# Kernel optimization log

Hardware: AMD Instinct MI355X
Metric: run time of the kernel (lower is better)

## Reference

```python
import jax, jax.numpy as jnp
import numpy as np

EMBED_DIM = 1024
N_HEADS = 16
HEAD_DIM = EMBED_DIM // N_HEADS
B, N = 4, 2048


def setup_inputs() -> dict:
    key = jax.random.key(0)
    k1, k2, k3, k4, k5 = jax.random.split(key, 5)
    x = jax.random.normal(k1, (B, N, EMBED_DIM), dtype=jnp.float32)
    # Per-head kqv Linear weights stacked: torch Linear(embed_dim, 3*head_dim)
    # torch stores weight as [out, in]; we store transposed [in, out] per head.
    scale = 1.0 / np.sqrt(EMBED_DIM)
    W_kqv = jax.random.uniform(k2, (N_HEADS, EMBED_DIM, 3 * HEAD_DIM), dtype=jnp.float32, minval=-scale, maxval=scale)
    b_kqv = jax.random.uniform(k3, (N_HEADS, 3 * HEAD_DIM), dtype=jnp.float32, minval=-scale, maxval=scale)
    W_proj = jax.random.uniform(k4, (EMBED_DIM, EMBED_DIM), dtype=jnp.float32, minval=-scale, maxval=scale)
    b_proj = jax.random.uniform(k5, (EMBED_DIM,), dtype=jnp.float32, minval=-scale, maxval=scale)
    return {"x": x, "W_kqv": W_kqv, "b_kqv": b_kqv, "W_proj": W_proj, "b_proj": b_proj}


def reference(x, W_kqv, b_kqv, W_proj, b_proj):
    Bx, Nx, D = x.shape
    H = W_kqv.shape[0]
    hd = W_kqv.shape[2] // 3
    # All per-head kqv projections at once: [B, H, N, 3*hd]
    kqv = jnp.einsum('bnd,hde->bhne', x, W_kqv) + b_kqv[None, :, None, :]
    # chunk order in source is (k, q, v)
    k, q, v = jnp.split(kqv, 3, axis=-1)
    # scores scaled by sqrt(head_dim) (D1 in attention_scores is head dim)
    scores = jnp.einsum('bhqd,bhkd->bhqk', q, k) / jnp.sqrt(jnp.float32(hd))
    causal = jnp.tril(jnp.ones((Nx, Nx), dtype=bool))  # [N, N]
    scores = jnp.where(causal[None, None, :, :], scores, -jnp.inf)
    attn = jax.nn.softmax(scores, axis=-1)
    sa = jnp.einsum('bhqk,bhkd->bhqd', attn, v)  # [B, H, N, hd]
    # concat heads along feature dim (head order preserved)
    sa = sa.transpose(0, 2, 1, 3).reshape(Bx, Nx, H * hd)
    # output projection: torch Linear with weight [out, in] -> y = sa @ W^T + b;
    # here W_proj is stored as [in, out]
    return sa @ W_proj + b_proj
```

## Files before the change

kernel.cpp:

```cpp
#include <hip/hip_runtime.h>
#include <math.h>

#define EMBED   1024
#define NHEADS  16
#define HD      64
#define BATCH   4
#define SEQ     2048
#define MROWS   (BATCH*SEQ)
#define NKV     8388608ull

typedef short short8 __attribute__((ext_vector_type(8)));
typedef float floatx4 __attribute__((ext_vector_type(4)));

__device__ __forceinline__ unsigned short f2b(float f) {
    union { float f; unsigned u; } v; v.f = f;
    unsigned r = v.u + 0x7FFFu + ((v.u >> 16) & 1u);
    return (unsigned short)(r >> 16);
}
__device__ __forceinline__ unsigned short f2b_fast(float f) {
    union { float f; unsigned u; } v; v.f = f;
    return (unsigned short)((v.u + 0x8000u) >> 16);
}

#define GLDS16(gp, lp) __builtin_amdgcn_global_load_lds( \
    (const __attribute__((address_space(1))) unsigned int*)(gp), \
    (__attribute__((address_space(3))) unsigned int*)(lp), 16, 0, 0)

__global__ __launch_bounds__(256) void convert_x(
    const float* __restrict__ x, unsigned short* __restrict__ x16)
{
    size_t idx = ((size_t)blockIdx.x * 256 + threadIdx.x) * 8;
    float4 a = *(const float4*)(x + idx);
    float4 b = *(const float4*)(x + idx + 4);
    ushort4 u0, u1;
    u0.x = f2b(a.x); u0.y = f2b(a.y); u0.z = f2b(a.z); u0.w = f2b(a.w);
    u1.x = f2b(b.x); u1.y = f2b(b.y); u1.z = f2b(b.z); u1.w = f2b(b.w);
    *(ushort4*)(x16 + idx) = u0;
    *(ushort4*)(x16 + idx + 4) = u1;
}

__global__ __launch_bounds__(256) void prep_wkqv(
    const float* __restrict__ Wk, unsigned short* __restrict__ Wt)
{
    __shared__ float tile[32][33];
    const int h = blockIdx.z;
    const int k0 = blockIdx.x * 32, e0 = blockIdx.y * 32;
    const float* inh = Wk + (size_t)h * 1024 * 192;
    const int tx = threadIdx.x & 31, ty = threadIdx.x >> 5;
    #pragma unroll
    for (int i = 0; i < 4; i++)
        tile[ty + i * 8][tx] = inh[(size_t)(k0 + ty + i * 8) * 192 + e0 + tx];
    __syncthreads();
    #pragma unroll
    for (int i = 0; i < 4; i++) {
        int e = e0 + ty + i * 8;
        int cp = (e >> 6) * 1024 + h * 64 + (e & 63);
        Wt[(size_t)cp * 1024 + k0 + tx] = f2b(tile[tx][ty + i * 8]);
    }
}

__global__ __launch_bounds__(256) void transpose_w(
    const float* __restrict__ in, unsigned short* __restrict__ outp, int R, int C)
{
    __shared__ float tile[32][33];
    const int r0 = blockIdx.x * 32, c0 = blockIdx.y * 32;
    const int tx = threadIdx.x & 31, ty = threadIdx.x >> 5;
    #pragma unroll
    for (int i = 0; i < 4; i++)
        tile[ty + i * 8][tx] = in[(size_t)(r0 + ty + i * 8) * C + c0 + tx];
    __syncthreads();
    #pragma unroll
    for (int i = 0; i < 4; i++)
        outp[(size_t)(c0 + ty + i * 8) * R + r0 + tx] = f2b(tile[tx][ty + i * 8]);
}

__global__ __launch_bounds__(256) void gemm_kqv(
    const unsigned short* __restrict__ A,
    const unsigned short* __restrict__ Bt,
    const float* __restrict__ bk,
    unsigned short* __restrict__ Kb16,
    unsigned short* __restrict__ Qb16,
    unsigned short* __restrict__ Vt16)
{
    __shared__ unsigned short smem[16384];
    unsigned short* As = smem;
    unsigned short* Bs = smem + 8192;

    const int mt = blockIdx.x;
    const int ct = blockIdx.y;
    const int t = threadIdx.x;
    const int wave = t >> 6, lane = t & 63;
    const int lr = lane & 15, quad = lane >> 4;
    const int wm = wave >> 1, wn = wave & 1;
    const int row0 = mt * 128, col0 = ct * 128;
    const int sr = lane >> 3, sc = lane & 7;

    floatx4 acc[4][4];
    #pragma unroll
    for (int a = 0; a < 4; a++)
        #pragma unroll
        for (int n = 0; n < 4; n++) acc[a][n] = (floatx4){0.f, 0.f, 0.f, 0.f};

    for (int k0 = 0; k0 < 1024; k0 += 64) {
        __syncthreads();
        #pragma unroll
        for (int i = 0; i < 4; i++) {
            int q = wave + i * 4;
            GLDS16(A  + (size_t)(row0 + q * 8 + sr) * 1024 + k0 + sc * 8, As + q * 512);
            GLDS16(Bt + (size_t)(col0 + q * 8 + sr) * 1024 + k0 + sc * 8, Bs + q * 512);
        }
        __syncthreads();
        #pragma unroll
        for (int kc = 0; kc < 2; kc++) {
            short8 af[4], bf[4];
            #pragma unroll
            for (int i = 0; i < 4; i++) {
                af[i] = *(const short8*)(As + (wm * 64 + i * 16 + lr) * 64 + kc * 32 + quad * 8);
                bf[i] = *(const short8*)(Bs + (wn * 64 + i * 16 + lr) * 64 + kc * 32 + quad * 8);
            }
            #pragma unroll
            for (int a = 0; a < 4; a++)
                #pragma unroll
                for (int n = 0; n < 4; n++)
                    acc[a][n] = __builtin_amdgcn_mfma_f32_16x16x32_bf16(af[a], bf[n], acc[a][n], 0, 0, 0);
        }
    }

    const int sec = ct >> 3;
    float bias[4];
    #pragma unroll
    for (int n = 0; n < 4; n++) {
        int c = col0 + wn * 64 + n * 16 + lr;
        int h = (c & 1023) >> 6;
        int e = sec * 64 + (c & 63);
        bias[n] = bk[h * 192 + e];
    }
    const int b = row0 >> 11;
    const int n0 = row0 & 2047;
    const float scl = (sec == 1) ? (0.125f * 1.44269504089f) : 1.0f;

    __syncthreads();
    if (sec < 2) {
        #pragma unroll
        for (int a = 0; a < 4; a++)
            #pragma unroll
            for (int n = 0; n < 4; n++) {
                int colS = (wn * 64 + n * 16 + lr) ^ (quad << 4);
                #pragma unroll
                for (int r = 0; r < 4; r++) {
                    int rw = wm * 64 + a * 16 + quad * 4 + r;
                    smem[rw * 128 + colS] = f2b((acc[a][n][r] + bias[n]) * scl);
                }
            }
        __syncthreads();
        unsigned short* dstbuf = (sec == 0) ? Kb16 : Qb16;
        const int rw = t >> 1, half = t & 1;
        const int h2 = (ct & 7) * 2 + half;
        const int s = (rw >> 2) & 3;
        unsigned short* dst = dstbuf + ((size_t)(b * 16 + h2) * 2048 + n0 + rw) * 64;
        #pragma unroll
        for (int u = 0; u < 8; u++) {
            int cg = half * 64 + ((u * 8) ^ (s << 4));
            *(float4*)(dst + u * 8) = *(const float4*)(&smem[rw * 128 + cg]);
        }
    } else {
        #pragma unroll
        for (int a = 0; a < 4; a++)
            #pragma unroll
            for (int n = 0; n < 4; n++) {
                int colv = wn * 64 + n * 16 + lr;
                int rowb = (wm * 64 + a * 16 + quad * 4) ^ ((colv & 7) << 3);
                ushort4 pk;
                pk.x = f2b(acc[a][n][0] + bias[n]);
                pk.y = f2b(acc[a][n][1] + bias[n]);
                pk.z = f2b(acc[a][n][2] + bias[n]);
                pk.w = f2b(acc[a][n][3] + bias[n]);
                *(ushort4*)(&smem[colv * 128 + rowb]) = pk;
            }
        __syncthreads();
        const int cg = t >> 1, hf = t & 1;
        const int d = cg & 63, h2 = (ct & 7) * 2 + (cg >> 6);
        unsigned short* dst = Vt16 + ((size_t)(b * 16 + h2) * 64 + d) * 2048 + n0 + hf * 64;
        #pragma unroll
        for (int u = 0; u < 8; u++) {
            int rr = hf * 64 + u * 8;
            int rs = rr ^ ((cg & 7) << 3);
            *(float4*)(dst + u * 8) = *(const float4*)(&smem[cg * 128 + rs]);
        }
    }
}

__global__ __launch_bounds__(256, 2) void attn_mfma(
    const unsigned short* __restrict__ Kb,
    const unsigned short* __restrict__ Qb,
    const unsigned short* __restrict__ Vt,
    unsigned short* __restrict__ sa)
{
    const int bx = blockIdx.x;
    const int bh = blockIdx.y;
    const int b = bh >> 4, h = bh & 15;
    const int wave = threadIdx.x >> 6;
    const int lane = threadIdx.x & 63;
    const int lr = lane & 15, quad = lane >> 4;
    const int qt_[2] = {bx, 15 - bx};

    __shared__ unsigned short Ks[64 * 64];
    __shared__ unsigned short Vs[64 * 64];
    __shared__ unsigned short Ps[4][2][16 * 72];

    const unsigned short* Kbh = Kb + (size_t)bh * 2048 * 64;
    const unsigned short* Vbh = Vt + (size_t)bh * 64 * 2048;
    const unsigned short* Qbh = Qb + (size_t)bh * 2048 * 64;

    short8 qf[2][2][2];
    #pragma unroll
    for (int tt = 0; tt < 2; tt++)
        #pragma unroll
        for (int s = 0; s < 2; s++) {
            const unsigned short* qp = Qbh +
                (size_t)(qt_[tt] * 128 + wave * 32 + s * 16 + lr) * 64 + quad * 8;
            qf[tt][s][0] = *(const short8*)(qp);
            qf[tt][s][1] = *(const short8*)(qp + 32);
        }

    floatx4 O[2][2][4];
    float ls[2][2][4];
    #pragma unroll
    for (int tt = 0; tt < 2; tt++)
        #pragma unroll
        for (int s = 0; s < 2; s++) {
            #pragma unroll
            for (int d = 0; d < 4; d++) O[tt][s][d] = (floatx4){0.f, 0.f, 0.f, 0.f};
            #pragma unroll
            for (int r = 0; r < 4; r++) ls[tt][s][r] = 0.f;
        }

    const int r_local = lane >> 3, cc = lane & 7;
    const int swz = cc ^ r_local;
    const int whalf = wave >> 1;

    const int ktmax = 2 * qt_[1] + 1;
    for (int kt = 0; kt <= ktmax; kt++) {
        const int k0 = kt * 64;
        __syncthreads();
        #pragma unroll
        for (int j = 0; j < 2; j++) {
            int R = wave * 16 + j * 8 + r_local;
            GLDS16(Kbh + (size_t)(k0 + R) * 64 + swz * 8, Ks + (wave * 16 + j * 8) * 64 + lane * 8);
            GLDS16(Vbh + (size_t)R * 2048 + k0 + swz * 8, Vs + (wave * 16 + j * 8) * 64 + lane * 8);
        }
        __syncthreads();

        #pragma unroll
        for (int tt = 0; tt < 2; tt++) {
            const int qt2 = qt_[tt];
            const int lim = 2 * qt2 + whalf;
            if (kt > lim) continue;

            floatx4 S[2][4];
            #pragma unroll
            for (int s = 0; s < 2; s++)
                #pragma unroll
                for (int a = 0; a < 4; a++) S[s][a] = (floatx4){0.f, 0.f, 0.f, 0.f};
            #pragma unroll
            for (int c = 0; c < 2; c++)
                #pragma unroll
                for (int a = 0; a < 4; a++) {
                    int R = a * 16 + lr;
                    short8 kf = *(const short8*)(Ks + R * 64 + (((c * 4 + quad) ^ (lr & 7)) * 8));
                    #pragma unroll
                    for (int s = 0; s < 2; s++)
                        S[s][a] = __builtin_amdgcn_mfma_f32_16x16x32_bf16(qf[tt][s][c], kf, S[s][a], 0, 0, 0);
                }

            if (kt == lim) {
                #pragma unroll
                for (int s = 0; s < 2; s++)
                    #pragma unroll
                    for (int a = 0; a < 4; a++) {
                        int col = k0 + a * 16 + lr;
                        #pragma unroll
                        for (int r = 0; r < 4; r++) {
                            int grow = qt2 * 128 + wave * 32 + s * 16 + quad * 4 + r;
                            if (col > grow) S[s][a][r] = -INFINITY;
                        }
                    }
            }

            #pragma unroll
            for (int s = 0; s < 2; s++)
                #pragma unroll
                for (int a = 0; a < 4; a++)
                    #pragma unroll
                    for (int r = 0; r < 4; r++) {
                        float p = __builtin_amdgcn_exp2f(S[s][a][r]);
                        ls[tt][s][r] += p;
                        Ps[wave][s][(quad * 4 + r) * 72 + a * 16 + lr] = f2b_fast(p);
                    }

            short8 pa[2][2];
            #pragma unroll
            for (int s = 0; s < 2; s++)
                #pragma unroll
                for (int c = 0; c < 2; c++)
                    pa[s][c] = *(const short8*)(Ps[wave][s] + lr * 72 + c * 32 + quad * 8);

            #pragma unroll
            for (int c = 0; c < 2; c++)
                #pragma unroll
                for (int d = 0; d < 4; d++) {
                    int R = d * 16 + lr;
                    short8 vf = *(const short8*)(Vs + R * 64 + (((c * 4 + quad) ^ (lr & 7)) * 8));
                    #pragma unroll
                    for (int s = 0; s < 2; s++)
                        O[tt][s][d] = __builtin_amdgcn_mfma_f32_16x16x32_bf16(pa[s][c], vf, O[tt][s][d], 0, 0, 0);
                }
        }
    }

    #pragma unroll
    for (int tt = 0; tt < 2; tt++)
        #pragma unroll
        for (int s = 0; s < 2; s++)
            #pragma unroll
            for (int r = 0; r < 4; r++) {
                float sm = ls[tt][s][r];
                sm += __shfl_xor(sm, 1);
                sm += __shfl_xor(sm, 2);
                sm += __shfl_xor(sm, 4);
                sm += __shfl_xor(sm, 8);
                float inv = 1.0f / sm;
                size_t base = ((size_t)(b * 2048 + qt_[tt] * 128 + wave * 32 + s * 16 + quad * 4 + r)) * 1024
                              + h * 64 + lr;
                #pragma unroll
                for (int d = 0; d < 4; d++)
                    sa[base + d * 16] = f2b(O[tt][s][d][r] * inv);
            }
}

__global__ __launch_bounds__(256) void gemm_proj(
    const unsigned short* __restrict__ A,
    const unsigned short* __restrict__ Bt,
    const float* __restrict__ bp,
    float* __restrict__ out)
{
    __shared__ unsigned short smem[16384];
    unsigned short* As = smem;
    unsigned short* Bs = smem + 8192;

    const int mt = blockIdx.x;
    const int ct = blockIdx.y;
    const int t = threadIdx.x;
    const int wave = t >> 6, lane = t & 63;
    const int lr = lane & 15, quad = lane >> 4;
    const int wm = wave >> 1, wn = wave & 1;
    const int row0 = mt * 128, col0 = ct * 128;
    const int sr = lane >> 3, sc = lane & 7;

    floatx4 acc[4][4];
    #pragma unroll
    for (int a = 0; a < 4; a++)
        #pragma unroll
        for (int n = 0; n < 4; n++) acc[a][n] = (floatx4){0.f, 0.f, 0.f, 0.f};

    for (int k0 = 0; k0 < 1024; k0 += 64) {
        __syncthreads();
        #pragma unroll
        for (int i = 0; i < 4; i++) {
            int q = wave + i * 4;
            GLDS16(A  + (size_t)(row0 + q * 8 + sr) * 1024 + k0 + sc * 8, As + q * 512);
            GLDS16(Bt + (size_t)(col0 + q * 8 + sr) * 1024 + k0 + sc * 8, Bs + q * 512);
        }
        __syncthreads();
        #pragma unroll
        for (int kc = 0; kc < 2; kc++) {
            short8 af[4], bf[4];
            #pragma unroll
            for (int i = 0; i < 4; i++) {
                af[i] = *(const short8*)(As + (wm * 64 + i * 16 + lr) * 64 + kc * 32 + quad * 8);
                bf[i] = *(const short8*)(Bs + (wn * 64 + i * 16 + lr) * 64 + kc * 32 + quad * 8);
            }
            #pragma unroll
            for (int a = 0; a < 4; a++)
                #pragma unroll
                for (int n = 0; n < 4; n++)
                    acc[a][n] = __builtin_amdgcn_mfma_f32_16x16x32_bf16(af[a], bf[n], acc[a][n], 0, 0, 0);
        }
    }

    float bias[4]; int cols[4];
    #pragma unroll
    for (int n = 0; n < 4; n++) {
        cols[n] = col0 + wn * 64 + n * 16 + lr;
        bias[n] = bp[cols[n]];
    }
    #pragma unroll
    for (int a = 0; a < 4; a++) {
        #pragma unroll
        for (int n = 0; n < 4; n++) {
            #pragma unroll
            for (int r = 0; r < 4; r++) {
                int m = row0 + wm * 64 + a * 16 + quad * 4 + r;
                out[(size_t)m * 1024 + cols[n]] = acc[a][n][r] + bias[n];
            }
        }
    }
}

extern "C" void kernel_launch(void* const* d_in, const int* in_sizes, int n_in,
                              void* d_out, int out_size, void* d_ws, size_t ws_size,
                              hipStream_t stream) {
    const float* x  = (const float*)d_in[0];
    const float* Wk = (const float*)d_in[1];
    const float* bk = (const float*)d_in[2];
    const float* Wp = (const float*)d_in[3];
    const float* bp = (const float*)d_in[4];
    float* out = (float*)d_out;

    unsigned short* Kb16 = (unsigned short*)d_ws;
    unsigned short* Qb16 = Kb16 + NKV;
    unsigned short* Vt16 = Qb16 + NKV;
    unsigned short* sa16 = Vt16 + NKV;
    unsigned short* x16  = sa16 + 8388608ull;
    unsigned short* Wt   = x16  + 8388608ull;
    unsigned short* Wpt  = Wt   + 3145728ull;

    convert_x<<<4096, 256, 0, stream>>>(x, x16);
    prep_wkqv<<<dim3(32, 6, 16), 256, 0, stream>>>(Wk, Wt);
    transpose_w<<<dim3(32, 32, 1), 256, 0, stream>>>(Wp, Wpt, 1024, 1024);
    gemm_kqv<<<dim3(64, 24), 256, 0, stream>>>(x16, Wt, bk, Kb16, Qb16, Vt16);
    attn_mfma<<<dim3(8, 64), 256, 0, stream>>>(Kb16, Qb16, Vt16, sa16);
    gemm_proj<<<dim3(64, 8), 256, 0, stream>>>(sa16, Wpt, bp, out);
}
```

Before: 275.7 us.

## Rewrite KQV GEMM with 256x256 tiles, double-buffered LDS and interleaved prefetch

The KQV projection GEMM moves from 128x128 tiles with 4 waves to 256x256 tiles with 8 waves. It double-buffers 128KB of LDS, with global-to-LDS prefetch of the next K slab interleaved across four MFMA phases, and uses setprio and explicit waitcnt/barriers. XOR swizzling on LDS reads is meant to avoid bank conflicts. The goal is more data reuse per tile and hiding load latency behind MFMA work. In exchange, the grid is much smaller (384 blocks) and the large LDS footprint limits occupancy. The epilogue is reorganized per wave for the K/Q and transposed V outputs.

```diff
diff --git a/kernel.cpp b/kernel.cpp
--- a/kernel.cpp
+++ b/kernel.cpp
@@ -74,7 +74,7 @@
         outp[(size_t)(c0 + ty + i * 8) * R + r0 + tx] = f2b(tile[tx][ty + i * 8]);
 }
 
-__global__ __launch_bounds__(256) void gemm_kqv(
+__global__ __launch_bounds__(512, 2) void gemm_kqv(
     const unsigned short* __restrict__ A,
     const unsigned short* __restrict__ Bt,
     const float* __restrict__ bk,
@@ -82,110 +82,180 @@
     unsigned short* __restrict__ Qb16,
     unsigned short* __restrict__ Vt16)
 {
-    __shared__ unsigned short smem[16384];
-    unsigned short* As = smem;
-    unsigned short* Bs = smem + 8192;
+    __shared__ unsigned short smem[65536];
 
     const int mt = blockIdx.x;
     const int ct = blockIdx.y;
     const int t = threadIdx.x;
     const int wave = t >> 6, lane = t & 63;
     const int lr = lane & 15, quad = lane >> 4;
-    const int wm = wave >> 1, wn = wave & 1;
-    const int row0 = mt * 128, col0 = ct * 128;
-    const int sr = lane >> 3, sc = lane & 7;
-
-    floatx4 acc[4][4];
-    #pragma unroll
-    for (int a = 0; a < 4; a++)
-        #pragma unroll
-        for (int n = 0; n < 4; n++) acc[a][n] = (floatx4){0.f, 0.f, 0.f, 0.f};
-
-    for (int k0 = 0; k0 < 1024; k0 += 64) {
-        __syncthreads();
-        #pragma unroll
-        for (int i = 0; i < 4; i++) {
-            int q = wave + i * 4;
-            GLDS16(A  + (size_t)(row0 + q * 8 + sr) * 1024 + k0 + sc * 8, As + q * 512);
-            GLDS16(Bt + (size_t)(col0 + q * 8 + sr) * 1024 + k0 + sc * 8, Bs + q * 512);
-        }
-        __syncthreads();
-        #pragma unroll
-        for (int kc = 0; kc < 2; kc++) {
-            short8 af[4], bf[4];
-            #pragma unroll
-            for (int i = 0; i < 4; i++) {
-                af[i] = *(const short8*)(As + (wm * 64 + i * 16 + lr) * 64 + kc * 32 + quad * 8);
-                bf[i] = *(const short8*)(Bs + (wn * 64 + i * 16 + lr) * 64 + kc * 32 + quad * 8);
-            }
-            #pragma unroll
-            for (int a = 0; a < 4; a++)
+    const int wr = wave >> 2, wc = wave & 3;
+    const int row0 = mt * 256, col0 = ct * 256;
+    const int swz8 = ((lane & 7) ^ ((lane >> 3) & 7)) * 8;
+    const int c0 = ((quad) ^ (lr & 7)) * 8;
+    const int c1 = ((4 + quad) ^ (lr & 7)) * 8;
+
+    floatx4 acc[8][4];
+    #pragma unroll
+    for (int m = 0; m < 8; m++)
+        #pragma unroll
+        for (int n = 0; n < 4; n++) acc[m][n] = (floatx4){0.f, 0.f, 0.f, 0.f};
+
+#define STG(G, R0, KC, L) do { \
+    _Pragma("unroll") \
+    for (int i_ = 0; i_ < 2; i_++) { \
+        int rl_ = i_ * 64 + wave * 8 + (lane >> 3); \
+        GLDS16((G) + (size_t)((R0) + rl_) * 1024 + (KC) + swz8, \
+               (L) + rl_ * 64 + (lane & 7) * 8); \
+    } } while (0)
+
+    STG(A,  row0,       0,  smem);
+    STG(A,  row0 + 128, 0,  smem + 8192);
+    STG(Bt, col0,       0,  smem + 16384);
+    STG(Bt, col0 + 128, 0,  smem + 16384 + 8192);
+    STG(Bt, col0,       64, smem + 32768 + 16384);
+    STG(Bt, col0 + 128, 64, smem + 32768 + 16384 + 8192);
+    asm volatile("s_waitcnt vmcnt(4)" ::: "memory");
+    __builtin_amdgcn_s_barrier();
+
+    #pragma unroll 2
+    for (int j = 0; j < 16; ++j) {
+        unsigned short* Ab = smem + (j & 1) * 32768;
+        unsigned short* Bb = Ab + 16384;
+        unsigned short* An = smem + ((j + 1) & 1) * 32768;
+        const unsigned short* pA = Ab + (wr * 128 + lr) * 64;
+        const unsigned short* pB = Bb + (wc * 64 + lr) * 64;
+
+        short8 b0[4], b1[4];
+
+        {
+            short8 af[4];
+            #pragma unroll
+            for (int m = 0; m < 4; m++) af[m] = *(const short8*)(pA + m * 1024 + c0);
+            #pragma unroll
+            for (int n = 0; n < 4; n++) b0[n] = *(const short8*)(pB + n * 1024 + c0);
+            if (j < 15) STG(A, row0, (j + 1) * 64, An);
+            __builtin_amdgcn_s_barrier();
+            asm volatile("s_waitcnt lgkmcnt(0)" ::: "memory");
+            __builtin_amdgcn_s_setprio(1);
+            #pragma unroll
+            for (int m = 0; m < 4; m++)
                 #pragma unroll
                 for (int n = 0; n < 4; n++)
-                    acc[a][n] = __builtin_amdgcn_mfma_f32_16x16x32_bf16(af[a], bf[n], acc[a][n], 0, 0, 0);
-        }
-    }
-
-    const int sec = ct >> 3;
+                    acc[m][n] = __builtin_amdgcn_mfma_f32_16x16x32_bf16(af[m], b0[n], acc[m][n], 0, 0, 0);
+            __builtin_amdgcn_s_setprio(0);
+            __builtin_amdgcn_s_barrier();
+        }
+        {
+            short8 af[4];
+            #pragma unroll
+            for (int m = 0; m < 4; m++) af[m] = *(const short8*)(pA + (m + 4) * 1024 + c0);
+            #pragma unroll
+            for (int n = 0; n < 4; n++) b1[n] = *(const short8*)(pB + n * 1024 + c1);
+            if (j < 15) STG(A, row0 + 128, (j + 1) * 64, An + 8192);
+            __builtin_amdgcn_s_barrier();
+            asm volatile("s_waitcnt lgkmcnt(0)" ::: "memory");
+            __builtin_amdgcn_s_setprio(1);
+            #pragma unroll
+            for (int m = 0; m < 4; m++)
+                #pragma unroll
+                for (int n = 0; n < 4; n++)
+                    acc[m + 4][n] = __builtin_amdgcn_mfma_f32_16x16x32_bf16(af[m], b0[n], acc[m + 4][n], 0, 0, 0);
+            __builtin_amdgcn_s_setprio(0);
+            __builtin_amdgcn_s_barrier();
+        }
+        {
+            short8 af[4];
+            #pragma unroll
+            for (int m = 0; m < 4; m++) af[m] = *(const short8*)(pA + m * 1024 + c1);
+            if (j < 14) STG(Bt, col0, (j + 2) * 64, Bb);
+            __builtin_amdgcn_s_barrier();
+            asm volatile("s_waitcnt lgkmcnt(0)" ::: "memory");
+            __builtin_amdgcn_s_setprio(1);
+            #pragma unroll
+            for (int m = 0; m < 4; m++)
+                #pragma unroll
+                for (int n = 0; n < 4; n++)
+                    acc[m][n] = __builtin_amdgcn_mfma_f32_16x16x32_bf16(af[m], b1[n], acc[m][n], 0, 0, 0);
+            __builtin_amdgcn_s_setprio(0);
+            __builtin_amdgcn_s_barrier();
+        }
+        {
+            short8 af[4];
+            #pragma unroll
+            for (int m = 0; m < 4; m++) af[m] = *(const short8*)(pA + (m + 4) * 1024 + c1);
+            if (j < 14) STG(Bt, col0 + 128, (j + 2) * 64, Bb + 8192);
+            __builtin_amdgcn_s_barrier();
+            asm volatile("s_waitcnt lgkmcnt(0)" ::: "memory");
+            __builtin_amdgcn_s_setprio(1);
+            #pragma unroll
+            for (int m = 0; m < 4; m++)
+                #pragma unroll
+                for (int n = 0; n < 4; n++)
+                    acc[m + 4][n] = __builtin_amdgcn_mfma_f32_16x16x32_bf16(af[m], b1[n], acc[m + 4][n], 0, 0, 0);
+            __builtin_amdgcn_s_setprio(0);
+            if (j < 14)       asm volatile("s_waitcnt vmcnt(4)" ::: "memory");
+            else if (j == 14) asm volatile("s_waitcnt vmcnt(0)" ::: "memory");
+            __builtin_amdgcn_s_barrier();
+        }
+    }
+#undef STG
+
+    unsigned short* W = smem + wave * 8192;
+    const int sec = ct >> 2;
+    const int h = ((ct & 3) << 2) + wc;
+    const int bidx = mt >> 3;
+    const int rbase = ((mt * 256) & 2047) + wr * 128;
+
     float bias[4];
     #pragma unroll
-    for (int n = 0; n < 4; n++) {
-        int c = col0 + wn * 64 + n * 16 + lr;
-        int h = (c & 1023) >> 6;
-        int e = sec * 64 + (c & 63);
-        bias[n] = bk[h * 192 + e];
-    }
-    const int b = row0 >> 11;
-    const int n0 = row0 & 2047;
-    const float scl = (sec == 1) ? (0.125f * 1.44269504089f) : 1.0f;
-
-    __syncthreads();
+    for (int n = 0; n < 4; n++) bias[n] = bk[h * 192 + sec * 64 + n * 16 + lr];
+
     if (sec < 2) {
-        #pragma unroll
-        for (int a = 0; a < 4; a++)
+        const float scl = (sec == 1) ? (0.125f * 1.44269504089f) : 1.0f;
+        #pragma unroll
+        for (int m = 0; m < 8; m++)
             #pragma unroll
             for (int n = 0; n < 4; n++) {
-                int colS = (wn * 64 + n * 16 + lr) ^ (quad << 4);
-                #pragma unroll
-                for (int r = 0; r < 4; r++) {
-                    int rw = wm * 64 + a * 16 + quad * 4 + r;
-                    smem[rw * 128 + colS] = f2b((acc[a][n][r] + bias[n]) * scl);
-                }
+                int es = (n * 16 + lr) ^ (quad << 4);
+                #pragma unroll
+                for (int r = 0; r < 4; r++)
+                    W[(m * 16 + quad * 4 + r) * 64 + es] = f2b((acc[m][n][r] + bias[n]) * scl);
             }
         __syncthreads();
-        unsigned short* dstbuf = (sec == 0) ? Kb16 : Qb16;
-        const int rw = t >> 1, half = t & 1;
-        const int h2 = (ct & 7) * 2 + half;
-        const int s = (rw >> 2) & 3;
-        unsigned short* dst = dstbuf + ((size_t)(b * 16 + h2) * 2048 + n0 + rw) * 64;
-        #pragma unroll
-        for (int u = 0; u < 8; u++) {
-            int cg = half * 64 + ((u * 8) ^ (s << 4));
-            *(float4*)(dst + u * 8) = *(const float4*)(&smem[rw * 128 + cg]);
+        unsigned short* dst = ((sec == 0) ? Kb16 : Qb16)
+                              + ((size_t)(bidx * 16 + h) * 2048 + rbase) * 64;
+        const int rrow = lane >> 3, chunk = lane & 7;
+        #pragma unroll
+        for (int p = 0; p < 16; p++) {
+            int row = p * 8 + rrow;
+            int ch = chunk ^ (((row >> 2) & 3) << 1);
+            *(float4*)(dst + (size_t)row * 64 + chunk * 8) =
+                *(const float4*)(W + row * 64 + ch * 8);
         }
     } else {
         #pragma unroll
-        for (int a = 0; a < 4; a++)
+        for (int m = 0; m < 8; m++)
             #pragma unroll
             for (int n = 0; n < 4; n++) {
-                int colv = wn * 64 + n * 16 + lr;
-                int rowb = (wm * 64 + a * 16 + quad * 4) ^ ((colv & 7) << 3);
+                int e = n * 16 + lr;
                 ushort4 pk;
-                pk.x = f2b(acc[a][n][0] + bias[n]);
-                pk.y = f2b(acc[a][n][1] + bias[n]);
-                pk.z = f2b(acc[a][n][2] + bias[n]);
-                pk.w = f2b(acc[a][n][3] + bias[n]);
-                *(ushort4*)(&smem[colv * 128 + rowb]) = pk;
+                pk.x = f2b(acc[m][n][0] + bias[n]);
+                pk.y = f2b(acc[m][n][1] + bias[n]);
+                pk.z = f2b(acc[m][n][2] + bias[n]);
+                pk.w = f2b(acc[m][n][3] + bias[n]);
+                int mp = m ^ (lr & 7);
+                *(ushort4*)(W + e * 128 + mp * 16 + quad * 4) = pk;
             }
         __syncthreads();
-        const int cg = t >> 1, hf = t & 1;
-        const int d = cg & 63, h2 = (ct & 7) * 2 + (cg >> 6);
-        unsigned short* dst = Vt16 + ((size_t)(b * 16 + h2) * 64 + d) * 2048 + n0 + hf * 64;
-        #pragma unroll
-        for (int u = 0; u < 8; u++) {
-            int rr = hf * 64 + u * 8;
-            int rs = rr ^ ((cg & 7) << 3);
-            *(float4*)(dst + u * 8) = *(const float4*)(&smem[cg * 128 + rs]);
+        unsigned short* dstV = Vt16 + (size_t)(bidx * 16 + h) * 64 * 2048 + rbase;
+        const int ev = lane >> 4, chunkR = lane & 15;
+        #pragma unroll
+        for (int p = 0; p < 16; p++) {
+            int e = p * 4 + ev;
+            int ch = chunkR ^ ((e & 7) << 1);
+            *(float4*)(dstV + (size_t)e * 2048 + chunkR * 8) =
+                *(const float4*)(W + e * 128 + ch * 8);
         }
     }
 }
@@ -428,7 +498,7 @@
     convert_x<<<4096, 256, 0, stream>>>(x, x16);
     prep_wkqv<<<dim3(32, 6, 16), 256, 0, stream>>>(Wk, Wt);
     transpose_w<<<dim3(32, 32, 1), 256, 0, stream>>>(Wp, Wpt, 1024, 1024);
-    gemm_kqv<<<dim3(64, 24), 256, 0, stream>>>(x16, Wt, bk, Kb16, Qb16, Vt16);
+    gemm_kqv<<<dim3(32, 12), 512, 0, stream>>>(x16, Wt, bk, Kb16, Qb16, Vt16);
     attn_mfma<<<dim3(8, 64), 256, 0, stream>>>(Kb16, Qb16, Vt16, sa16);
     gemm_proj<<<dim3(64, 8), 256, 0, stream>>>(sa16, Wpt, bp, out);
 }
```

Result: faster. 254.1 us (-7.8%).
